# Optimization experiments

Hardware: AMD Instinct MI355X
Metric: run time of the kernel (lower is better)

## Reference

```python
import jax, jax.numpy as jnp
import numpy as np
from jax import lax

H = W = 128          # feature map size (gen_line_map uses 128x128)
C = 128              # dim_loi
NPTS0 = 32           # n_pts0 samples per line
NPTS1 = 8            # after MaxPool1d(4, stride=4)
TOPK = 50            # n_dyn_junc
SCALE = 5.0          # proposal_lines distance scale


def proposal_lines(md_maps, dis_maps, scale=SCALE):
    h, w = md_maps.shape[1], md_maps.shape[2]
    y0, x0 = jnp.meshgrid(jnp.arange(h, dtype=jnp.float32),
                          jnp.arange(w, dtype=jnp.float32), indexing='ij')
    md_ = (md_maps[0] - 0.5) * np.pi * 2
    st_ = md_maps[1] * np.pi / 2
    ed_ = -md_maps[2] * np.pi / 2
    cs_md, ss_md = jnp.cos(md_), jnp.sin(md_)
    cs_st = jnp.clip(jnp.cos(st_), 0.001, None)
    ss_st = jnp.clip(jnp.sin(st_), 0.001, None)
    cs_ed = jnp.clip(jnp.cos(ed_), 0.001, None)
    ss_ed = jnp.clip(jnp.sin(ed_), None, -0.001)
    y_st = ss_st / cs_st
    y_ed = ss_ed / cs_ed
    d = dis_maps[0] * scale
    x_st = (cs_md - ss_md * y_st) * d
    y_s = (ss_md + cs_md * y_st) * d
    x_ed = (cs_md - ss_md * y_ed) * d
    y_e = (ss_md + cs_md * y_ed) * d
    x_st_f = jnp.clip(x_st + x0, 0.0, w - 1)
    y_st_f = jnp.clip(y_s + y0, 0.0, h - 1)
    x_ed_f = jnp.clip(x_ed + x0, 0.0, w - 1)
    y_ed_f = jnp.clip(y_e + y0, 0.0, h - 1)
    return jnp.stack((x_st_f, y_st_f, x_ed_f, y_ed_f), axis=-1).reshape(-1, 4)


def pooling(feats, lines):
    # feats: [C, H, W]; lines: [N, 4]
    h, w = feats.shape[1], feats.shape[2]
    tspan = jnp.linspace(0.0, 1.0, NPTS0)[None, None, :]           # [1,1,32]
    U, V = lines[:, :2], lines[:, 2:]
    sp = U[:, :, None] * tspan + V[:, :, None] * (1 - tspan) - 0.5  # [N,2,32]
    sp = sp.transpose(0, 2, 1).reshape(-1, 2)                       # [N*32, 2]
    px, py = sp[:, 0], sp[:, 1]
    px0 = jnp.clip(jnp.floor(px), 0.0, w - 1)
    py0 = jnp.clip(jnp.floor(py), 0.0, h - 1)
    px1 = jnp.clip(px0 + 1, 0.0, w - 1)
    py1 = jnp.clip(py0 + 1, 0.0, h - 1)
    px0l, py0l = px0.astype(jnp.int32), py0.astype(jnp.int32)
    px1l, py1l = px1.astype(jnp.int32), py1.astype(jnp.int32)
    # bilinear gather-weight, fused in a single expression: [C, N*32]
    xp = (feats[:, py0l, px0l] * (py1 - py) * (px1 - px)
          + feats[:, py1l, px0l] * (py - py0) * (px1 - px)
          + feats[:, py0l, px1l] * (py1 - py) * (px - px0)
          + feats[:, py1l, px1l] * (py - py0) * (px - px0))
    xp = xp.reshape(C, -1, NPTS0).transpose(1, 0, 2)                # [N, C, 32]
    xp = xp.reshape(xp.shape[0], C, NPTS1, NPTS0 // NPTS1).max(-1)  # MaxPool1d(4,4)
    return xp.reshape(-1, NPTS1 * C)                                # [N, 1024]


def nms(a):
    # F.max_pool2d(a, 3, stride=1, padding=1) then keep local maxima
    ap = lax.reduce_window(a, -jnp.inf, lax.max, (1, 3, 3), (1, 1, 1), 'SAME')
    return a * (a == ap).astype(a.dtype)


def get_junctions(jloc_nms, joff, topk=TOPK):
    h, w = jloc_nms.shape[1], jloc_nms.shape[2]
    scores, index = lax.top_k(jloc_nms.reshape(-1), topk)
    jf = joff.reshape(2, -1)
    y = (index // w).astype(jnp.float32) + jf[1][index] + 0.5
    x = (index % w).astype(jnp.float32) + jf[0][index] + 0.5
    juncs = jnp.stack((x, y), axis=1)                               # [topk, 2]
    return juncs, scores, index


def setup_inputs() -> dict:
    key = jax.random.key(0)
    ks = jax.random.split(key, 12)
    return {
        'md': jax.random.uniform(ks[0], (3, H, W), dtype=jnp.float32),
        'dis': jax.random.uniform(ks[1], (1, H, W), dtype=jnp.float32),
        'res': jax.random.uniform(ks[2], (1, H, W), dtype=jnp.float32),
        'jloc': jax.random.uniform(ks[3], (1, H, W), dtype=jnp.float32),
        'joff': jax.random.uniform(ks[4], (2, H, W), dtype=jnp.float32) - 0.5,
        'feats': jax.random.normal(ks[5], (C, H, W), dtype=jnp.float32),
        'W1': jax.random.normal(ks[6], (1024, C * NPTS1), dtype=jnp.float32) * 0.02,
        'b1': jax.random.normal(ks[7], (1024,), dtype=jnp.float32) * 0.02,
        'W2': jax.random.normal(ks[8], (1024, 1024), dtype=jnp.float32) * 0.02,
        'b2': jax.random.normal(ks[9], (1024,), dtype=jnp.float32) * 0.02,
        'W3': jax.random.normal(ks[10], (1, 1024), dtype=jnp.float32) * 0.02,
        'b3': jax.random.normal(ks[11], (1,), dtype=jnp.float32) * 0.02,
    }


def reference(md, dis, res, jloc, joff, feats, W1, b1, W2, b2, W3, b3):
    # line proposals at 3 residual scales (use_residual=True)
    lines = jnp.concatenate([
        proposal_lines(md, dis + s * res) for s in (-1.0, 0.0, 1.0)
    ], axis=0)                                                      # [3*H*W, 4]
    # LOI bilinear pooling + scoring MLP (self.fc)
    x = pooling(feats, lines)                                       # [N, 1024]
    x = jax.nn.relu(x @ W1.T + b1)
    x = jax.nn.relu(x @ W2.T + b2)
    logits = x @ W3.T + b3                                          # [N, 1]
    # junction decode: NMS + topk + offset gather
    juncs, jscores, _ = get_junctions(nms(jloc), joff, TOPK)
    return logits, juncs, jscores
```

## Files before the change

kernel.cpp:

```cpp
#include <hip/hip_runtime.h>
#include <hip/hip_bf16.h>
#include <math.h>

#define HH 128
#define WW 128
#define HW 16384
#define NL 49152
#define CC 128
#define NPTS0 32
#define NPTS1 8
#define PI_F 3.14159265358979323846f

typedef __attribute__((ext_vector_type(8))) short short8;
typedef __attribute__((ext_vector_type(4))) float f32x4;

__device__ __forceinline__ ushort f2bf(float f) {
    unsigned u = __builtin_bit_cast(unsigned, f);
    unsigned rounding = 0x7FFFu + ((u >> 16) & 1u);
    return (ushort)((u + rounding) >> 16);
}

__device__ __forceinline__ void gload_lds16(const void* gsrc, void* ldst) {
    __builtin_amdgcn_global_load_lds(
        (const __attribute__((address_space(1))) unsigned int*)gsrc,
        (__attribute__((address_space(3))) unsigned int*)ldst,
        16, 0, 0);
}

__device__ __forceinline__ void unpk8(uint4 d, float* f) {
    f[0] = __builtin_bit_cast(float, d.x << 16);
    f[1] = __builtin_bit_cast(float, d.x & 0xFFFF0000u);
    f[2] = __builtin_bit_cast(float, d.y << 16);
    f[3] = __builtin_bit_cast(float, d.y & 0xFFFF0000u);
    f[4] = __builtin_bit_cast(float, d.z << 16);
    f[5] = __builtin_bit_cast(float, d.z & 0xFFFF0000u);
    f[6] = __builtin_bit_cast(float, d.w << 16);
    f[7] = __builtin_bit_cast(float, d.w & 0xFFFF0000u);
}

__global__ __launch_bounds__(256) void k_lines(
    const float* __restrict__ md, const float* __restrict__ dis,
    const float* __restrict__ res, float* __restrict__ lines)
{
    int g = blockIdx.x * 256 + threadIdx.x;
    if (g >= NL) return;
    int s = g / HW;
    int pix = g - s * HW;
    float sf = (float)(s - 1);
    int y = pix >> 7, x = pix & 127;

    float md0 = md[pix], md1 = md[HW + pix], md2 = md[2 * HW + pix];
    float d = (dis[pix] + sf * res[pix]) * 5.0f;

    float md_ = (md0 - 0.5f) * (2.0f * PI_F);
    float st_ = md1 * (0.5f * PI_F);
    float ed_ = -md2 * (0.5f * PI_F);
    float cs_md = cosf(md_), ss_md = sinf(md_);
    float cs_st = fmaxf(cosf(st_), 0.001f);
    float ss_st = fmaxf(sinf(st_), 0.001f);
    float cs_ed = fmaxf(cosf(ed_), 0.001f);
    float ss_ed = fminf(sinf(ed_), -0.001f);
    float y_st = ss_st / cs_st;
    float y_ed = ss_ed / cs_ed;
    float x_st = (cs_md - ss_md * y_st) * d;
    float y_s  = (ss_md + cs_md * y_st) * d;
    float x_ed = (cs_md - ss_md * y_ed) * d;
    float y_e  = (ss_md + cs_md * y_ed) * d;

    float4 o;
    o.x = fminf(fmaxf(x_st + (float)x, 0.0f), 127.0f);
    o.y = fminf(fmaxf(y_s  + (float)y, 0.0f), 127.0f);
    o.z = fminf(fmaxf(x_ed + (float)x, 0.0f), 127.0f);
    o.w = fminf(fmaxf(y_e  + (float)y, 0.0f), 127.0f);
    ((float4*)lines)[g] = o;
}

__global__ void k_transpose(const float* __restrict__ in, ushort* __restrict__ out)
{
    __shared__ float tile[32][33];
    int cb = blockIdx.x;
    int pb = blockIdx.y;
    int tx = threadIdx.x, ty = threadIdx.y;
#pragma unroll
    for (int j = 0; j < 32; j += 8)
        tile[ty + j][tx] = in[(size_t)(cb * 32 + ty + j) * HW + pb * 32 + tx];
    __syncthreads();
#pragma unroll
    for (int j = 0; j < 32; j += 8)
        out[(size_t)(pb * 32 + ty + j) * CC + cb * 32 + tx] = f2bf(tile[tx][ty + j]);
}

__global__ void k_cvt(const float* __restrict__ a, const float* __restrict__ b,
                      ushort* __restrict__ oa, ushort* __restrict__ ob, int n)
{
    int i = blockIdx.x * 256 + threadIdx.x;
    if (i < n) { oa[i] = f2bf(a[i]); ob[i] = f2bf(b[i]); }
}

__global__ __launch_bounds__(128, 2) void k_pool(
    const ushort* __restrict__ ft, const float* __restrict__ lines,
    ushort* __restrict__ X)
{
    __shared__ __align__(16) unsigned smeta[2048];
    const int t = threadIdx.x;
    const int l_loc = t >> 4, c8 = t & 15;
    const int gl0 = blockIdx.x * 8;

#pragma unroll
    for (int e = 0; e < 2; ++e) {
        int s = t + e * 128;
        int ml = s >> 5, sp = s & 31;
        float4 L = ((const float4*)lines)[gl0 + ml];
        float tf = (float)sp * (1.0f / 31.0f);
        float omt = 1.0f - tf;
        float px = L.x * tf + L.z * omt - 0.5f;
        float py = L.y * tf + L.w * omt - 0.5f;
        float px0 = fminf(fmaxf(floorf(px), 0.0f), 127.0f);
        float py0 = fminf(fmaxf(floorf(py), 0.0f), 127.0f);
        float px1 = fminf(px0 + 1.0f, 127.0f);
        float py1 = fminf(py0 + 1.0f, 127.0f);
        int ix0 = (int)px0, iy0 = (int)py0, ix1 = (int)px1, iy1 = (int)py1;
        float4 wv;
        wv.x = (py1 - py) * (px1 - px);
        wv.y = (py  - py0) * (px1 - px);
        wv.z = (py1 - py) * (px  - px0);
        wv.w = (py  - py0) * (px  - px0);
        int o00 = (iy0 * WW + ix0) * (CC * 2);
        int dx  = (ix1 - ix0) * (CC * 2);
        int dy  = (iy1 - iy0) * (WW * CC * 2);
        int4 ov;
        ov.x = o00;
        ov.y = o00 + dy;
        ov.z = o00 + dx;
        ov.w = o00 + dy + dx;
        *(float4*)&smeta[s * 8]     = wv;
        *(int4*)  &smeta[s * 8 + 4] = ov;
    }
    __syncthreads();

    const unsigned coff = (unsigned)(c8 * 16);
    const char* fbase = (const char*)ft;
    float m[8][8];
#pragma unroll
    for (int ch = 0; ch < 8; ++ch)
#pragma unroll
        for (int g = 0; g < 8; ++g) m[ch][g] = -INFINITY;

#pragma unroll
    for (int g = 0; g < 8; ++g) {
#pragma unroll
        for (int j = 0; j < 4; ++j) {
            const unsigned* mp = &smeta[(l_loc * 32 + g * 4 + j) * 8];
            float4 wv = *(const float4*)mp;
            int4  ov = *(const int4*)(mp + 4);
            uint4 d00 = *(const uint4*)(fbase + ((unsigned)ov.x + coff));
            uint4 d10 = *(const uint4*)(fbase + ((unsigned)ov.y + coff));
            uint4 d01 = *(const uint4*)(fbase + ((unsigned)ov.z + coff));
            uint4 d11 = *(const uint4*)(fbase + ((unsigned)ov.w + coff));
            float f00[8], f10[8], f01[8], f11[8];
            unpk8(d00, f00); unpk8(d10, f10); unpk8(d01, f01); unpk8(d11, f11);
#pragma unroll
            for (int ch = 0; ch < 8; ++ch) {
                float v = f00[ch] * wv.x + f10[ch] * wv.y
                        + f01[ch] * wv.z + f11[ch] * wv.w;
                m[ch][g] = fmaxf(m[ch][g], v);
            }
        }
    }

    ushort* Xp = X + (size_t)(gl0 + l_loc) * 1024 + c8 * 64;
#pragma unroll
    for (int ch = 0; ch < 8; ++ch) {
        short8 pk;
#pragma unroll
        for (int g = 0; g < 8; ++g) pk[g] = (short)f2bf(m[ch][g]);
        *(short8*)(Xp + ch * 8) = pk;
    }
}

#define NIT 8
template<int EPI>
__global__ __launch_bounds__(1024) void k_gemm2(
    const ushort* __restrict__ A, const ushort* __restrict__ B,
    const float* __restrict__ bias, ushort* __restrict__ Y,
    const float* __restrict__ w3, float* __restrict__ logits,
    int M, int N, int K)
{
    __shared__ __align__(16) ushort lds[65536];
    const int tid = threadIdx.x;
    const int w = tid >> 6, l = tid & 63;
    const int lr = l & 15, kq = l >> 4;
    const int wm = w >> 2, wn = w & 3;

    const int nwg = gridDim.x;
    const int cpx = nwg >> 3;
    const int swzb = (blockIdx.x & 7) * cpx + (blockIdx.x >> 3);
    const int nbn = N >> 8;
    const int m_blk = swzb / nbn;
    const int n_blk = swzb % nbn;
    const int m0 = m_blk << 8, n0 = n_blk << 8;

    const ushort* pA = A + (size_t)m0 * K;
    const ushort* pB = B + (size_t)n0 * K;

    const int rS = tid >> 3;
    const int gS = (tid & 7) ^ (rS & 7);

#define STG(gp, rowoff, kt, regbase) \
    gload_lds16((gp) + (size_t)((rowoff) + rS) * K + (kt) * 64 + gS * 8, \
                &lds[(regbase) + tid * 8]);

#define FBAR { __builtin_amdgcn_sched_barrier(0); __builtin_amdgcn_s_barrier(); \
               __builtin_amdgcn_sched_barrier(0); }

    const int swz0 = ((kq) ^ (lr & 7)) * 8;
    const int swz1 = ((4 + kq) ^ (lr & 7)) * 8;
    int aoff[4], boff[4];
#pragma unroll
    for (int m = 0; m < 4; ++m) aoff[m] = (wm * 64 + m * 16 + lr) * 64;
#pragma unroll
    for (int n = 0; n < 4; ++n) boff[n] = 16384 + (wn * 64 + n * 16 + lr) * 64;

    f32x4 acc[4][4] = {};
    short8 bq0, bq1, bq2, bq3;

#define MF8(MLO, A0, A1) \
    acc[MLO+0][0] = __builtin_amdgcn_mfma_f32_16x16x32_bf16(bq0, A0, acc[MLO+0][0], 0, 0, 0); \
    acc[MLO+0][1] = __builtin_amdgcn_mfma_f32_16x16x32_bf16(bq1, A0, acc[MLO+0][1], 0, 0, 0); \
    acc[MLO+0][2] = __builtin_amdgcn_mfma_f32_16x16x32_bf16(bq2, A0, acc[MLO+0][2], 0, 0, 0); \
    acc[MLO+0][3] = __builtin_amdgcn_mfma_f32_16x16x32_bf16(bq3, A0, acc[MLO+0][3], 0, 0, 0); \
    acc[MLO+1][0] = __builtin_amdgcn_mfma_f32_16x16x32_bf16(bq0, A1, acc[MLO+1][0], 0, 0, 0); \
    acc[MLO+1][1] = __builtin_amdgcn_mfma_f32_16x16x32_bf16(bq1, A1, acc[MLO+1][1], 0, 0, 0); \
    acc[MLO+1][2] = __builtin_amdgcn_mfma_f32_16x16x32_bf16(bq2, A1, acc[MLO+1][2], 0, 0, 0); \
    acc[MLO+1][3] = __builtin_amdgcn_mfma_f32_16x16x32_bf16(bq3, A1, acc[MLO+1][3], 0, 0, 0);

    STG(pA, 0,   0, 0);
    STG(pA, 128, 0, 8192);
    STG(pB, 0,   0, 16384);
    STG(pB, 128, 0, 24576);
    STG(pB, 0,   1, 49152);
    asm volatile("s_waitcnt vmcnt(1)" ::: "memory");
    FBAR;

    for (int i = 0; i < NIT; ++i) {
        const int t1 = 2 * i + 1, t2 = 2 * i + 2, t3 = 2 * i + 3;
        const bool pf = (i < NIT - 1);

        bq0 = *(const short8*)&lds[boff[0] + swz0];
        bq1 = *(const short8*)&lds[boff[1] + swz0];
        bq2 = *(const short8*)&lds[boff[2] + swz0];
        bq3 = *(const short8*)&lds[boff[3] + swz0];
        {
            short8 a0 = *(const short8*)&lds[aoff[0] + swz0];
            short8 a1 = *(const short8*)&lds[aoff[1] + swz0];
            STG(pB, 128, t1, 57344);
            FBAR;
            __builtin_amdgcn_s_setprio(1); MF8(0, a0, a1) __builtin_amdgcn_s_setprio(0);
            FBAR;
        }
        {
            short8 a2 = *(const short8*)&lds[aoff[2] + swz0];
            short8 a3 = *(const short8*)&lds[aoff[3] + swz0];
            STG(pA, 0, t1, 32768);
            FBAR;
            __builtin_amdgcn_s_setprio(1); MF8(2, a2, a3) __builtin_amdgcn_s_setprio(0);
            FBAR;
        }
        bq0 = *(const short8*)&lds[boff[0] + swz1];
        bq1 = *(const short8*)&lds[boff[1] + swz1];
        bq2 = *(const short8*)&lds[boff[2] + swz1];
        bq3 = *(const short8*)&lds[boff[3] + swz1];
        {
            short8 a0 = *(const short8*)&lds[aoff[0] + swz1];
            short8 a1 = *(const short8*)&lds[aoff[1] + swz1];
            STG(pA, 128, t1, 40960);
            FBAR;
            __builtin_amdgcn_s_setprio(1); MF8(0, a0, a1) __builtin_amdgcn_s_setprio(0);
            FBAR;
        }
        {
            short8 a2 = *(const short8*)&lds[aoff[2] + swz1];
            short8 a3 = *(const short8*)&lds[aoff[3] + swz1];
            if (pf) STG(pB, 0, t2, 16384);
            FBAR;
            __builtin_amdgcn_s_setprio(1); MF8(2, a2, a3) __builtin_amdgcn_s_setprio(0);
            if (pf) { asm volatile("s_waitcnt vmcnt(1)" ::: "memory"); }
            else    { asm volatile("s_waitcnt vmcnt(0)" ::: "memory"); }
            FBAR;
        }
        bq0 = *(const short8*)&lds[32768 + boff[0] + swz0];
        bq1 = *(const short8*)&lds[32768 + boff[1] + swz0];
        bq2 = *(const short8*)&lds[32768 + boff[2] + swz0];
        bq3 = *(const short8*)&lds[32768 + boff[3] + swz0];
        {
            short8 a0 = *(const short8*)&lds[32768 + aoff[0] + swz0];
            short8 a1 = *(const short8*)&lds[32768 + aoff[1] + swz0];
            if (pf) STG(pB, 128, t2, 24576);
            FBAR;
            __builtin_amdgcn_s_setprio(1); MF8(0, a0, a1) __builtin_amdgcn_s_setprio(0);
            FBAR;
        }
        {
            short8 a2 = *(const short8*)&lds[32768 + aoff[2] + swz0];
            short8 a3 = *(const short8*)&lds[32768 + aoff[3] + swz0];
            if (pf) STG(pA, 0, t2, 0);
            FBAR;
            __builtin_amdgcn_s_setprio(1); MF8(2, a2, a3) __builtin_amdgcn_s_setprio(0);
            FBAR;
        }
        bq0 = *(const short8*)&lds[32768 + boff[0] + swz1];
        bq1 = *(const short8*)&lds[32768 + boff[1] + swz1];
        bq2 = *(const short8*)&lds[32768 + boff[2] + swz1];
        bq3 = *(const short8*)&lds[32768 + boff[3] + swz1];
        {
            short8 a0 = *(const short8*)&lds[32768 + aoff[0] + swz1];
            short8 a1 = *(const short8*)&lds[32768 + aoff[1] + swz1];
            if (pf) STG(pA, 128, t2, 8192);
            FBAR;
            __builtin_amdgcn_s_setprio(1); MF8(0, a0, a1) __builtin_amdgcn_s_setprio(0);
            FBAR;
        }
        {
            short8 a2 = *(const short8*)&lds[32768 + aoff[2] + swz1];
            short8 a3 = *(const short8*)&lds[32768 + aoff[3] + swz1];
            if (pf) STG(pB, 0, t3, 49152);
            FBAR;
            __builtin_amdgcn_s_setprio(1); MF8(2, a2, a3) __builtin_amdgcn_s_setprio(0);
            if (pf) { asm volatile("s_waitcnt vmcnt(1)" ::: "memory"); }
            FBAR;
        }
    }
#undef STG
#undef FBAR
#undef MF8

    if (EPI == 0) {
#pragma unroll
        for (int n = 0; n < 4; ++n) {
            int cbase = n0 + wn * 64 + n * 16 + kq * 4;
            float4 bv4 = *(const float4*)&bias[cbase];
#pragma unroll
            for (int m = 0; m < 4; ++m) {
                int row = m0 + wm * 64 + m * 16 + lr;
                ushort4 pk;
                pk.x = f2bf(fmaxf(acc[m][n][0] + bv4.x, 0.0f));
                pk.y = f2bf(fmaxf(acc[m][n][1] + bv4.y, 0.0f));
                pk.z = f2bf(fmaxf(acc[m][n][2] + bv4.z, 0.0f));
                pk.w = f2bf(fmaxf(acc[m][n][3] + bv4.w, 0.0f));
                *(ushort4*)(Y + (size_t)row * N + cbase) = pk;
            }
        }
    } else {
        float4 bv4[4], w34[4];
#pragma unroll
        for (int n = 0; n < 4; ++n) {
            int cbase = n0 + wn * 64 + n * 16 + kq * 4;
            bv4[n] = *(const float4*)&bias[cbase];
            w34[n] = *(const float4*)&w3[cbase];
        }
#pragma unroll
        for (int m = 0; m < 4; ++m) {
            float s = 0.0f;
#pragma unroll
            for (int n = 0; n < 4; ++n) {
                s += fmaxf(acc[m][n][0] + bv4[n].x, 0.0f) * w34[n].x;
                s += fmaxf(acc[m][n][1] + bv4[n].y, 0.0f) * w34[n].y;
                s += fmaxf(acc[m][n][2] + bv4[n].z, 0.0f) * w34[n].z;
                s += fmaxf(acc[m][n][3] + bv4[n].w, 0.0f) * w34[n].w;
            }
            s += __shfl_xor(s, 16, 64);
            s += __shfl_xor(s, 32, 64);
            if (kq == 0)
                atomicAdd(&logits[m0 + wm * 64 + m * 16 + lr], s);
        }
    }
}

__global__ void k_init_logits(float* __restrict__ logits, const float* __restrict__ b3, int n)
{
    int i = blockIdx.x * 256 + threadIdx.x;
    if (i < n) logits[i] = b3[0];
}

__global__ __launch_bounds__(256) void k_nms_topk(
    const float* __restrict__ jloc, unsigned long long* __restrict__ cand)
{
    __shared__ unsigned long long sk[256];
    const int t = threadIdx.x;
    const int idx = blockIdx.x * 256 + t;
    const int y = idx >> 7, x = idx & 127;
    float cv = jloc[idx];
    float m = cv;
    for (int dy = -1; dy <= 1; ++dy) {
        int yy = y + dy;
        if (yy < 0 || yy > 127) continue;
        for (int dx = -1; dx <= 1; ++dx) {
            int xx = x + dx;
            if (xx < 0 || xx > 127) continue;
            m = fmaxf(m, jloc[(yy << 7) + xx]);
        }
    }
    float nv = (cv == m) ? cv : 0.0f;
    unsigned vb = __builtin_bit_cast(unsigned, nv);
    sk[t] = ((unsigned long long)vb << 32) | (unsigned)(0xFFFFFFFFu - idx);
    __syncthreads();
    for (int k = 2; k <= 256; k <<= 1) {
        for (int j = k >> 1; j >= 1; j >>= 1) {
            int ixj = t ^ j;
            if (ixj > t) {
                unsigned long long a = sk[t], b = sk[ixj];
                bool up = ((t & k) == 0);
                if (up ? (a < b) : (a > b)) { sk[t] = b; sk[ixj] = a; }
            }
            __syncthreads();
        }
    }
    if (t < 64) cand[blockIdx.x * 64 + t] = (t < 50) ? sk[t] : 0ull;
}

__global__ __launch_bounds__(1024) void k_topk_final(
    const unsigned long long* __restrict__ cand,
    const float* __restrict__ joff, float* __restrict__ outj)
{
    __shared__ unsigned long long sk[4096];
    const int t = threadIdx.x;
#pragma unroll
    for (int e = 0; e < 4; ++e) sk[t + (e << 10)] = cand[t + (e << 10)];
    __syncthreads();
    for (int k = 2; k <= 4096; k <<= 1) {
        for (int j = k >> 1; j >= 1; j >>= 1) {
#pragma unroll
            for (int e = 0; e < 4; ++e) {
                int i = t + (e << 10);
                int ixj = i ^ j;
                if (ixj > i) {
                    unsigned long long a = sk[i], b = sk[ixj];
                    bool up = ((i & k) == 0);
                    if (up ? (a < b) : (a > b)) { sk[i] = b; sk[ixj] = a; }
                }
            }
            __syncthreads();
        }
    }
    if (t < 50) {
        unsigned long long kk = sk[t];
        unsigned idx = 0xFFFFFFFFu - (unsigned)(kk & 0xFFFFFFFFull);
        float val = __builtin_bit_cast(float, (unsigned)(kk >> 32));
        int y = idx >> 7, x = idx & 127;
        outj[2 * t]     = (float)x + joff[idx]      + 0.5f;
        outj[2 * t + 1] = (float)y + joff[HW + idx] + 0.5f;
        outj[100 + t]   = val;
    }
}

extern "C" void kernel_launch(void* const* d_in, const int* in_sizes, int n_in,
                              void* d_out, int out_size, void* d_ws, size_t ws_size,
                              hipStream_t stream) {
    const float* md   = (const float*)d_in[0];
    const float* dis  = (const float*)d_in[1];
    const float* res  = (const float*)d_in[2];
    const float* jloc = (const float*)d_in[3];
    const float* joff = (const float*)d_in[4];
    const float* feats= (const float*)d_in[5];
    const float* W1   = (const float*)d_in[6];
    const float* b1   = (const float*)d_in[7];
    const float* W2   = (const float*)d_in[8];
    const float* b2   = (const float*)d_in[9];
    const float* W3   = (const float*)d_in[10];
    const float* b3   = (const float*)d_in[11];
    float* out = (float*)d_out;

    char* ws = (char*)d_ws;
    size_t off = 0;
    auto alloc = [&](size_t bytes) {
        void* p = ws + off;
        off = (off + bytes + 255) & ~(size_t)255;
        return p;
    };
    float*  lines = (float*) alloc((size_t)NL * 4 * sizeof(float));
    ushort* ft    = (ushort*)alloc((size_t)HW * CC * 2);
    ushort* W1b   = (ushort*)alloc((size_t)1024 * 1024 * 2);
    ushort* W2b   = (ushort*)alloc((size_t)1024 * 1024 * 2);
    ushort* X     = (ushort*)alloc((size_t)NL * 1024 * 2);
    ushort* Y1    = (ushort*)alloc((size_t)NL * 1024 * 2);
    unsigned long long* cand = (unsigned long long*)alloc(4096 * 8);

    k_lines<<<NL / 256, 256, 0, stream>>>(md, dis, res, lines);
    k_transpose<<<dim3(CC / 32, HW / 32), dim3(32, 8), 0, stream>>>(feats, ft);
    k_cvt<<<(1024 * 1024) / 256, 256, 0, stream>>>(W1, W2, W1b, W2b, 1024 * 1024);
    k_pool<<<NL / 8, 128, 0, stream>>>(ft, lines, X);

    int ngrid = (NL / 256) * (1024 / 256);
    k_gemm2<0><<<ngrid, 1024, 0, stream>>>(X, W1b, b1, Y1, nullptr, nullptr, NL, 1024, 1024);
    k_init_logits<<<NL / 256, 256, 0, stream>>>(out, b3, NL);
    k_gemm2<1><<<ngrid, 1024, 0, stream>>>(Y1, W2b, b2, nullptr, W3, out, NL, 1024, 1024);

    k_nms_topk<<<64, 256, 0, stream>>>(jloc, cand);
    k_topk_final<<<1, 1024, 0, stream>>>(cand, joff, out + NL);
}
```

Before: 384.4 us.

## Switch GEMM to 32x32x16 MFMA with 8 waves and 128x64 per-wave tiles

Reworks the two large MLP GEMMs to use 512-thread blocks with 32x32x16 bf16 MFMA instead of 1024 threads with 16x16x32. Each wave now computes a 128x64 output sub-tile, so every LDS fragment read feeds more MFMA work and fewer LDS reads are needed per FLOP. Staging issues two global-to-LDS loads per thread, and the waitcnt thresholds and epilogue index mapping are adjusted to match. Register pressure per wave rises, and the logits init launch is moved to the start of the stream.

```diff
diff --git a/kernel.cpp b/kernel.cpp
--- a/kernel.cpp
+++ b/kernel.cpp
@@ -13,6 +13,7 @@
 
 typedef __attribute__((ext_vector_type(8))) short short8;
 typedef __attribute__((ext_vector_type(4))) float f32x4;
+typedef __attribute__((ext_vector_type(16))) float f32x16;
 
 __device__ __forceinline__ ushort f2bf(float f) {
     unsigned u = __builtin_bit_cast(unsigned, f);
@@ -180,7 +181,7 @@
 
 #define NIT 8
 template<int EPI>
-__global__ __launch_bounds__(1024) void k_gemm2(
+__global__ __launch_bounds__(512, 1) void k_gemm2(
     const ushort* __restrict__ A, const ushort* __restrict__ B,
     const float* __restrict__ bias, ushort* __restrict__ Y,
     const float* __restrict__ w3, float* __restrict__ logits,
@@ -189,7 +190,8 @@
     __shared__ __align__(16) ushort lds[65536];
     const int tid = threadIdx.x;
     const int w = tid >> 6, l = tid & 63;
-    const int lr = l & 15, kq = l >> 4;
+    const int lr = l & 31;
+    const int lh = l >> 5;
     const int wm = w >> 2, wn = w & 3;
 
     const int nwg = gridDim.x;
@@ -206,172 +208,203 @@
     const int rS = tid >> 3;
     const int gS = (tid & 7) ^ (rS & 7);
 
-#define STG(gp, rowoff, kt, regbase) \
-    gload_lds16((gp) + (size_t)((rowoff) + rS) * K + (kt) * 64 + gS * 8, \
-                &lds[(regbase) + tid * 8]);
+#define STG_A(tt, rowoff, regbase) { \
+    gload_lds16(pA + (size_t)((rowoff) + rS) * K + (tt) * 64 + gS * 8, \
+                &lds[(regbase) + tid * 8]); \
+    gload_lds16(pA + (size_t)((rowoff) + 64 + rS) * K + (tt) * 64 + gS * 8, \
+                &lds[(regbase) + 4096 + tid * 8]); }
+#define STG_B(tt, rowoff, regbase) { \
+    gload_lds16(pB + (size_t)((rowoff) + rS) * K + (tt) * 64 + gS * 8, \
+                &lds[(regbase) + tid * 8]); \
+    gload_lds16(pB + (size_t)((rowoff) + 64 + rS) * K + (tt) * 64 + gS * 8, \
+                &lds[(regbase) + 4096 + tid * 8]); }
 
 #define FBAR { __builtin_amdgcn_sched_barrier(0); __builtin_amdgcn_s_barrier(); \
                __builtin_amdgcn_sched_barrier(0); }
 
-    const int swz0 = ((kq) ^ (lr & 7)) * 8;
-    const int swz1 = ((4 + kq) ^ (lr & 7)) * 8;
-    int aoff[4], boff[4];
-#pragma unroll
-    for (int m = 0; m < 4; ++m) aoff[m] = (wm * 64 + m * 16 + lr) * 64;
-#pragma unroll
-    for (int n = 0; n < 4; ++n) boff[n] = 16384 + (wn * 64 + n * 16 + lr) * 64;
-
-    f32x4 acc[4][4] = {};
-    short8 bq0, bq1, bq2, bq3;
-
-#define MF8(MLO, A0, A1) \
-    acc[MLO+0][0] = __builtin_amdgcn_mfma_f32_16x16x32_bf16(bq0, A0, acc[MLO+0][0], 0, 0, 0); \
-    acc[MLO+0][1] = __builtin_amdgcn_mfma_f32_16x16x32_bf16(bq1, A0, acc[MLO+0][1], 0, 0, 0); \
-    acc[MLO+0][2] = __builtin_amdgcn_mfma_f32_16x16x32_bf16(bq2, A0, acc[MLO+0][2], 0, 0, 0); \
-    acc[MLO+0][3] = __builtin_amdgcn_mfma_f32_16x16x32_bf16(bq3, A0, acc[MLO+0][3], 0, 0, 0); \
-    acc[MLO+1][0] = __builtin_amdgcn_mfma_f32_16x16x32_bf16(bq0, A1, acc[MLO+1][0], 0, 0, 0); \
-    acc[MLO+1][1] = __builtin_amdgcn_mfma_f32_16x16x32_bf16(bq1, A1, acc[MLO+1][1], 0, 0, 0); \
-    acc[MLO+1][2] = __builtin_amdgcn_mfma_f32_16x16x32_bf16(bq2, A1, acc[MLO+1][2], 0, 0, 0); \
-    acc[MLO+1][3] = __builtin_amdgcn_mfma_f32_16x16x32_bf16(bq3, A1, acc[MLO+1][3], 0, 0, 0);
-
-    STG(pA, 0,   0, 0);
-    STG(pA, 128, 0, 8192);
-    STG(pB, 0,   0, 16384);
-    STG(pB, 128, 0, 24576);
-    STG(pB, 0,   1, 49152);
-    asm volatile("s_waitcnt vmcnt(1)" ::: "memory");
+    int gsw[4];
+#pragma unroll
+    for (int ks = 0; ks < 4; ++ks) gsw[ks] = ((ks * 2 + lh) ^ (l & 7)) * 8;
+    int aoff[4], boff[2];
+#pragma unroll
+    for (int mt = 0; mt < 4; ++mt) aoff[mt] = (wm * 128 + mt * 32 + lr) * 64;
+#pragma unroll
+    for (int nt = 0; nt < 2; ++nt) boff[nt] = 16384 + (wn * 64 + nt * 32 + lr) * 64;
+
+    f32x16 acc[4][2] = {};
+    short8 bqA0, bqA1, bqB0, bqB1;
+
+#define MF8(B0, B1, A0, A1, A2, A3) \
+    acc[0][0] = __builtin_amdgcn_mfma_f32_32x32x16_bf16(B0, A0, acc[0][0], 0, 0, 0); \
+    acc[0][1] = __builtin_amdgcn_mfma_f32_32x32x16_bf16(B1, A0, acc[0][1], 0, 0, 0); \
+    acc[1][0] = __builtin_amdgcn_mfma_f32_32x32x16_bf16(B0, A1, acc[1][0], 0, 0, 0); \
+    acc[1][1] = __builtin_amdgcn_mfma_f32_32x32x16_bf16(B1, A1, acc[1][1], 0, 0, 0); \
+    acc[2][0] = __builtin_amdgcn_mfma_f32_32x32x16_bf16(B0, A2, acc[2][0], 0, 0, 0); \
+    acc[2][1] = __builtin_amdgcn_mfma_f32_32x32x16_bf16(B1, A2, acc[2][1], 0, 0, 0); \
+    acc[3][0] = __builtin_amdgcn_mfma_f32_32x32x16_bf16(B0, A3, acc[3][0], 0, 0, 0); \
+    acc[3][1] = __builtin_amdgcn_mfma_f32_32x32x16_bf16(B1, A3, acc[3][1], 0, 0, 0);
+
+    STG_A(0, 0,   0);
+    STG_A(0, 128, 8192);
+    STG_B(0, 0,   16384);
+    STG_B(0, 128, 24576);
+    STG_B(1, 0,   49152);
+    asm volatile("s_waitcnt vmcnt(2)" ::: "memory");
     FBAR;
 
     for (int i = 0; i < NIT; ++i) {
         const int t1 = 2 * i + 1, t2 = 2 * i + 2, t3 = 2 * i + 3;
         const bool pf = (i < NIT - 1);
 
-        bq0 = *(const short8*)&lds[boff[0] + swz0];
-        bq1 = *(const short8*)&lds[boff[1] + swz0];
-        bq2 = *(const short8*)&lds[boff[2] + swz0];
-        bq3 = *(const short8*)&lds[boff[3] + swz0];
-        {
-            short8 a0 = *(const short8*)&lds[aoff[0] + swz0];
-            short8 a1 = *(const short8*)&lds[aoff[1] + swz0];
-            STG(pB, 128, t1, 57344);
-            FBAR;
-            __builtin_amdgcn_s_setprio(1); MF8(0, a0, a1) __builtin_amdgcn_s_setprio(0);
-            FBAR;
-        }
-        {
-            short8 a2 = *(const short8*)&lds[aoff[2] + swz0];
-            short8 a3 = *(const short8*)&lds[aoff[3] + swz0];
-            STG(pA, 0, t1, 32768);
-            FBAR;
-            __builtin_amdgcn_s_setprio(1); MF8(2, a2, a3) __builtin_amdgcn_s_setprio(0);
-            FBAR;
-        }
-        bq0 = *(const short8*)&lds[boff[0] + swz1];
-        bq1 = *(const short8*)&lds[boff[1] + swz1];
-        bq2 = *(const short8*)&lds[boff[2] + swz1];
-        bq3 = *(const short8*)&lds[boff[3] + swz1];
-        {
-            short8 a0 = *(const short8*)&lds[aoff[0] + swz1];
-            short8 a1 = *(const short8*)&lds[aoff[1] + swz1];
-            STG(pA, 128, t1, 40960);
-            FBAR;
-            __builtin_amdgcn_s_setprio(1); MF8(0, a0, a1) __builtin_amdgcn_s_setprio(0);
-            FBAR;
-        }
-        {
-            short8 a2 = *(const short8*)&lds[aoff[2] + swz1];
-            short8 a3 = *(const short8*)&lds[aoff[3] + swz1];
-            if (pf) STG(pB, 0, t2, 16384);
-            FBAR;
-            __builtin_amdgcn_s_setprio(1); MF8(2, a2, a3) __builtin_amdgcn_s_setprio(0);
-            if (pf) { asm volatile("s_waitcnt vmcnt(1)" ::: "memory"); }
+        bqA0 = *(const short8*)&lds[boff[0] + gsw[0]];
+        bqA1 = *(const short8*)&lds[boff[1] + gsw[0]];
+        bqB0 = *(const short8*)&lds[boff[0] + gsw[1]];
+        bqB1 = *(const short8*)&lds[boff[1] + gsw[1]];
+        {
+            short8 a0 = *(const short8*)&lds[aoff[0] + gsw[0]];
+            short8 a1 = *(const short8*)&lds[aoff[1] + gsw[0]];
+            short8 a2 = *(const short8*)&lds[aoff[2] + gsw[0]];
+            short8 a3 = *(const short8*)&lds[aoff[3] + gsw[0]];
+            STG_B(t1, 128, 57344);
+            FBAR;
+            __builtin_amdgcn_s_setprio(1); MF8(bqA0, bqA1, a0, a1, a2, a3) __builtin_amdgcn_s_setprio(0);
+            FBAR;
+        }
+        {
+            short8 a0 = *(const short8*)&lds[aoff[0] + gsw[1]];
+            short8 a1 = *(const short8*)&lds[aoff[1] + gsw[1]];
+            short8 a2 = *(const short8*)&lds[aoff[2] + gsw[1]];
+            short8 a3 = *(const short8*)&lds[aoff[3] + gsw[1]];
+            STG_A(t1, 0, 32768);
+            FBAR;
+            __builtin_amdgcn_s_setprio(1); MF8(bqB0, bqB1, a0, a1, a2, a3) __builtin_amdgcn_s_setprio(0);
+            FBAR;
+        }
+        bqA0 = *(const short8*)&lds[boff[0] + gsw[2]];
+        bqA1 = *(const short8*)&lds[boff[1] + gsw[2]];
+        bqB0 = *(const short8*)&lds[boff[0] + gsw[3]];
+        bqB1 = *(const short8*)&lds[boff[1] + gsw[3]];
+        {
+            short8 a0 = *(const short8*)&lds[aoff[0] + gsw[2]];
+            short8 a1 = *(const short8*)&lds[aoff[1] + gsw[2]];
+            short8 a2 = *(const short8*)&lds[aoff[2] + gsw[2]];
+            short8 a3 = *(const short8*)&lds[aoff[3] + gsw[2]];
+            STG_A(t1, 128, 40960);
+            FBAR;
+            __builtin_amdgcn_s_setprio(1); MF8(bqA0, bqA1, a0, a1, a2, a3) __builtin_amdgcn_s_setprio(0);
+            FBAR;
+        }
+        {
+            short8 a0 = *(const short8*)&lds[aoff[0] + gsw[3]];
+            short8 a1 = *(const short8*)&lds[aoff[1] + gsw[3]];
+            short8 a2 = *(const short8*)&lds[aoff[2] + gsw[3]];
+            short8 a3 = *(const short8*)&lds[aoff[3] + gsw[3]];
+            if (pf) STG_B(t2, 0, 16384);
+            FBAR;
+            __builtin_amdgcn_s_setprio(1); MF8(bqB0, bqB1, a0, a1, a2, a3) __builtin_amdgcn_s_setprio(0);
+            if (pf) { asm volatile("s_waitcnt vmcnt(2)" ::: "memory"); }
             else    { asm volatile("s_waitcnt vmcnt(0)" ::: "memory"); }
             FBAR;
         }
-        bq0 = *(const short8*)&lds[32768 + boff[0] + swz0];
-        bq1 = *(const short8*)&lds[32768 + boff[1] + swz0];
-        bq2 = *(const short8*)&lds[32768 + boff[2] + swz0];
-        bq3 = *(const short8*)&lds[32768 + boff[3] + swz0];
-        {
-            short8 a0 = *(const short8*)&lds[32768 + aoff[0] + swz0];
-            short8 a1 = *(const short8*)&lds[32768 + aoff[1] + swz0];
-            if (pf) STG(pB, 128, t2, 24576);
-            FBAR;
-            __builtin_amdgcn_s_setprio(1); MF8(0, a0, a1) __builtin_amdgcn_s_setprio(0);
-            FBAR;
-        }
-        {
-            short8 a2 = *(const short8*)&lds[32768 + aoff[2] + swz0];
-            short8 a3 = *(const short8*)&lds[32768 + aoff[3] + swz0];
-            if (pf) STG(pA, 0, t2, 0);
-            FBAR;
-            __builtin_amdgcn_s_setprio(1); MF8(2, a2, a3) __builtin_amdgcn_s_setprio(0);
-            FBAR;
-        }
-        bq0 = *(const short8*)&lds[32768 + boff[0] + swz1];
-        bq1 = *(const short8*)&lds[32768 + boff[1] + swz1];
-        bq2 = *(const short8*)&lds[32768 + boff[2] + swz1];
-        bq3 = *(const short8*)&lds[32768 + boff[3] + swz1];
-        {
-            short8 a0 = *(const short8*)&lds[32768 + aoff[0] + swz1];
-            short8 a1 = *(const short8*)&lds[32768 + aoff[1] + swz1];
-            if (pf) STG(pA, 128, t2, 8192);
-            FBAR;
-            __builtin_amdgcn_s_setprio(1); MF8(0, a0, a1) __builtin_amdgcn_s_setprio(0);
-            FBAR;
-        }
-        {
-            short8 a2 = *(const short8*)&lds[32768 + aoff[2] + swz1];
-            short8 a3 = *(const short8*)&lds[32768 + aoff[3] + swz1];
-            if (pf) STG(pB, 0, t3, 49152);
-            FBAR;
-            __builtin_amdgcn_s_setprio(1); MF8(2, a2, a3) __builtin_amdgcn_s_setprio(0);
-            if (pf) { asm volatile("s_waitcnt vmcnt(1)" ::: "memory"); }
-            FBAR;
-        }
-    }
-#undef STG
+        bqA0 = *(const short8*)&lds[32768 + boff[0] + gsw[0]];
+        bqA1 = *(const short8*)&lds[32768 + boff[1] + gsw[0]];
+        bqB0 = *(const short8*)&lds[32768 + boff[0] + gsw[1]];
+        bqB1 = *(const short8*)&lds[32768 + boff[1] + gsw[1]];
+        {
+            short8 a0 = *(const short8*)&lds[32768 + aoff[0] + gsw[0]];
+            short8 a1 = *(const short8*)&lds[32768 + aoff[1] + gsw[0]];
+            short8 a2 = *(const short8*)&lds[32768 + aoff[2] + gsw[0]];
+            short8 a3 = *(const short8*)&lds[32768 + aoff[3] + gsw[0]];
+            if (pf) STG_B(t2, 128, 24576);
+            FBAR;
+            __builtin_amdgcn_s_setprio(1); MF8(bqA0, bqA1, a0, a1, a2, a3) __builtin_amdgcn_s_setprio(0);
+            FBAR;
+        }
+        {
+            short8 a0 = *(const short8*)&lds[32768 + aoff[0] + gsw[1]];
+            short8 a1 = *(const short8*)&lds[32768 + aoff[1] + gsw[1]];
+            short8 a2 = *(const short8*)&lds[32768 + aoff[2] + gsw[1]];
+            short8 a3 = *(const short8*)&lds[32768 + aoff[3] + gsw[1]];
+            if (pf) STG_A(t2, 0, 0);
+            FBAR;
+            __builtin_amdgcn_s_setprio(1); MF8(bqB0, bqB1, a0, a1, a2, a3) __builtin_amdgcn_s_setprio(0);
+            FBAR;
+        }
+        bqA0 = *(const short8*)&lds[32768 + boff[0] + gsw[2]];
+        bqA1 = *(const short8*)&lds[32768 + boff[1] + gsw[2]];
+        bqB0 = *(const short8*)&lds[32768 + boff[0] + gsw[3]];
+        bqB1 = *(const short8*)&lds[32768 + boff[1] + gsw[3]];
+        {
+            short8 a0 = *(const short8*)&lds[32768 + aoff[0] + gsw[2]];
+            short8 a1 = *(const short8*)&lds[32768 + aoff[1] + gsw[2]];
+            short8 a2 = *(const short8*)&lds[32768 + aoff[2] + gsw[2]];
+            short8 a3 = *(const short8*)&lds[32768 + aoff[3] + gsw[2]];
+            if (pf) STG_A(t2, 128, 8192);
+            FBAR;
+            __builtin_amdgcn_s_setprio(1); MF8(bqA0, bqA1, a0, a1, a2, a3) __builtin_amdgcn_s_setprio(0);
+            FBAR;
+        }
+        {
+            short8 a0 = *(const short8*)&lds[32768 + aoff[0] + gsw[3]];
+            short8 a1 = *(const short8*)&lds[32768 + aoff[1] + gsw[3]];
+            short8 a2 = *(const short8*)&lds[32768 + aoff[2] + gsw[3]];
+            short8 a3 = *(const short8*)&lds[32768 + aoff[3] + gsw[3]];
+            if (pf) STG_B(t3, 0, 49152);
+            FBAR;
+            __builtin_amdgcn_s_setprio(1); MF8(bqB0, bqB1, a0, a1, a2, a3) __builtin_amdgcn_s_setprio(0);
+            if (pf) { asm volatile("s_waitcnt vmcnt(2)" ::: "memory"); }
+            FBAR;
+        }
+    }
+#undef STG_A
+#undef STG_B
 #undef FBAR
 #undef MF8
 
     if (EPI == 0) {
 #pragma unroll
-        for (int n = 0; n < 4; ++n) {
-            int cbase = n0 + wn * 64 + n * 16 + kq * 4;
-            float4 bv4 = *(const float4*)&bias[cbase];
-#pragma unroll
-            for (int m = 0; m < 4; ++m) {
-                int row = m0 + wm * 64 + m * 16 + lr;
-                ushort4 pk;
-                pk.x = f2bf(fmaxf(acc[m][n][0] + bv4.x, 0.0f));
-                pk.y = f2bf(fmaxf(acc[m][n][1] + bv4.y, 0.0f));
-                pk.z = f2bf(fmaxf(acc[m][n][2] + bv4.z, 0.0f));
-                pk.w = f2bf(fmaxf(acc[m][n][3] + bv4.w, 0.0f));
-                *(ushort4*)(Y + (size_t)row * N + cbase) = pk;
+        for (int mt = 0; mt < 4; ++mt) {
+            int row = m0 + wm * 128 + mt * 32 + lr;
+#pragma unroll
+            for (int nt = 0; nt < 2; ++nt) {
+#pragma unroll
+                for (int q = 0; q < 4; ++q) {
+                    int cbase = n0 + wn * 64 + nt * 32 + q * 8 + lh * 4;
+                    float4 bv4 = *(const float4*)&bias[cbase];
+                    ushort4 pk;
+                    pk.x = f2bf(fmaxf(acc[mt][nt][q * 4 + 0] + bv4.x, 0.0f));
+                    pk.y = f2bf(fmaxf(acc[mt][nt][q * 4 + 1] + bv4.y, 0.0f));
+                    pk.z = f2bf(fmaxf(acc[mt][nt][q * 4 + 2] + bv4.z, 0.0f));
+                    pk.w = f2bf(fmaxf(acc[mt][nt][q * 4 + 3] + bv4.w, 0.0f));
+                    *(ushort4*)(Y + (size_t)row * N + cbase) = pk;
+                }
             }
         }
     } else {
-        float4 bv4[4], w34[4];
-#pragma unroll
-        for (int n = 0; n < 4; ++n) {
-            int cbase = n0 + wn * 64 + n * 16 + kq * 4;
-            bv4[n] = *(const float4*)&bias[cbase];
-            w34[n] = *(const float4*)&w3[cbase];
-        }
-#pragma unroll
-        for (int m = 0; m < 4; ++m) {
+        float4 bv4[2][4], w34[2][4];
+#pragma unroll
+        for (int nt = 0; nt < 2; ++nt)
+#pragma unroll
+            for (int q = 0; q < 4; ++q) {
+                int cbase = n0 + wn * 64 + nt * 32 + q * 8 + lh * 4;
+                bv4[nt][q] = *(const float4*)&bias[cbase];
+                w34[nt][q] = *(const float4*)&w3[cbase];
+            }
+#pragma unroll
+        for (int mt = 0; mt < 4; ++mt) {
             float s = 0.0f;
 #pragma unroll
-            for (int n = 0; n < 4; ++n) {
-                s += fmaxf(acc[m][n][0] + bv4[n].x, 0.0f) * w34[n].x;
-                s += fmaxf(acc[m][n][1] + bv4[n].y, 0.0f) * w34[n].y;
-                s += fmaxf(acc[m][n][2] + bv4[n].z, 0.0f) * w34[n].z;
-                s += fmaxf(acc[m][n][3] + bv4[n].w, 0.0f) * w34[n].w;
-            }
-            s += __shfl_xor(s, 16, 64);
+            for (int nt = 0; nt < 2; ++nt)
+#pragma unroll
+                for (int q = 0; q < 4; ++q) {
+                    s += fmaxf(acc[mt][nt][q * 4 + 0] + bv4[nt][q].x, 0.0f) * w34[nt][q].x;
+                    s += fmaxf(acc[mt][nt][q * 4 + 1] + bv4[nt][q].y, 0.0f) * w34[nt][q].y;
+                    s += fmaxf(acc[mt][nt][q * 4 + 2] + bv4[nt][q].z, 0.0f) * w34[nt][q].z;
+                    s += fmaxf(acc[mt][nt][q * 4 + 3] + bv4[nt][q].w, 0.0f) * w34[nt][q].w;
+                }
             s += __shfl_xor(s, 32, 64);
-            if (kq == 0)
-                atomicAdd(&logits[m0 + wm * 64 + m * 16 + lr], s);
+            if (lh == 0)
+                atomicAdd(&logits[m0 + wm * 128 + mt * 32 + lr], s);
         }
     }
 }
@@ -485,15 +518,15 @@
     ushort* Y1    = (ushort*)alloc((size_t)NL * 1024 * 2);
     unsigned long long* cand = (unsigned long long*)alloc(4096 * 8);
 
+    k_init_logits<<<NL / 256, 256, 0, stream>>>(out, b3, NL);
     k_lines<<<NL / 256, 256, 0, stream>>>(md, dis, res, lines);
     k_transpose<<<dim3(CC / 32, HW / 32), dim3(32, 8), 0, stream>>>(feats, ft);
     k_cvt<<<(1024 * 1024) / 256, 256, 0, stream>>>(W1, W2, W1b, W2b, 1024 * 1024);
     k_pool<<<NL / 8, 128, 0, stream>>>(ft, lines, X);
 
     int ngrid = (NL / 256) * (1024 / 256);
-    k_gemm2<0><<<ngrid, 1024, 0, stream>>>(X, W1b, b1, Y1, nullptr, nullptr, NL, 1024, 1024);
-    k_init_logits<<<NL / 256, 256, 0, stream>>>(out, b3, NL);
-    k_gemm2<1><<<ngrid, 1024, 0, stream>>>(Y1, W2b, b2, nullptr, W3, out, NL, 1024, 1024);
+    k_gemm2<0><<<ngrid, 512, 0, stream>>>(X, W1b, b1, Y1, nullptr, nullptr, NL, 1024, 1024);
+    k_gemm2<1><<<ngrid, 512, 0, stream>>>(Y1, W2b, b2, nullptr, W3, out, NL, 1024, 1024);
 
     k_nms_topk<<<64, 256, 0, stream>>>(jloc, cand);
     k_topk_final<<<1, 1024, 0, stream>>>(cand, joff, out + NL);
```

New measurement: 380.3 us. About the same (-1.1%).
